# Optimization experiments

Hardware: AMD Instinct MI355X
Metric: run time of the kernel (lower is better)

Reference implementation:

```python
import jax, jax.numpy as jnp
import numpy as np

# Model dims
C = 16          # in_channels / d_model
D_INNER = 64    # expand * C, expand = 64 // C = 4
HEADDIM = 4
NHEADS = D_INNER // HEADDIM   # 16
D_STATE = 64
D_CONV = 4
CONV_DIM = D_INNER + 2 * D_STATE        # 192 (x, B, C streams)
D_IN_PROJ = 2 * D_INNER + 2 * D_STATE + NHEADS  # 272 (z, xBC, dt)
# Input volume
BSZ, DD, HH, WW = 8, 32, 16, 16
L = DD * HH * WW  # 8192, multiple of 256 -> exact adaptive max pool
POOL = 256


def setup_inputs():
    key = jax.random.key(0)
    ks = jax.random.split(key, 10)
    x = jax.random.normal(ks[0], (BSZ, C, DD, HH, WW), jnp.float32)
    # 3 independent Mamba2 blocks -> stack params with leading dim 3
    Win = jax.random.normal(ks[1], (3, D_IN_PROJ, C), jnp.float32) / np.sqrt(C).astype(np.float32)
    conv_w = jax.random.normal(ks[2], (3, CONV_DIM, D_CONV), jnp.float32) / np.sqrt(D_CONV).astype(np.float32)
    conv_b = jax.random.normal(ks[3], (3, CONV_DIM), jnp.float32) * 0.1
    dt_bias = jax.random.normal(ks[4], (3, NHEADS), jnp.float32) * 0.5
    A_log = jnp.log(jax.random.uniform(ks[5], (3, NHEADS), jnp.float32, minval=1.0, maxval=16.0))
    Dp = jax.random.normal(ks[6], (3, NHEADS), jnp.float32) * 0.5 + 1.0
    norm_w = jnp.ones((3, D_INNER), jnp.float32)
    Wout = jax.random.normal(ks[7], (3, C, D_INNER), jnp.float32) / np.sqrt(D_INNER).astype(np.float32)
    gamma = jnp.ones((3, C), jnp.float32)
    beta = jnp.zeros((3, C), jnp.float32)
    lin_w = jax.random.normal(ks[8], (3, 1, C), jnp.float32) / np.sqrt(C).astype(np.float32)
    lin_b = jnp.zeros((3, 1), jnp.float32)
    return dict(x=x, Win=Win, conv_w=conv_w, conv_b=conv_b, dt_bias=dt_bias,
                A_log=A_log, Dp=Dp, norm_w=norm_w, Wout=Wout,
                gamma=gamma, beta=beta, lin_w=lin_w, lin_b=lin_b)


def _mamba2(u, Win, conv_w, conv_b, dt_bias, A_log, Dp, norm_w, Wout):
    """Mamba2 block: u (B, L, C) -> (B, L, C). ngroups=1, rmsnorm gated."""
    B, Lx, _ = u.shape
    zxbcdt = jnp.einsum('blc,pc->blp', u, Win)  # (B, L, 272)
    z = zxbcdt[..., :D_INNER]
    xBC = zxbcdt[..., D_INNER:D_INNER + CONV_DIM]
    dt = jax.nn.softplus(zxbcdt[..., D_INNER + CONV_DIM:] + dt_bias)  # (B, L, H)
    # causal depthwise conv over time
    conv = jax.lax.conv_general_dilated(
        jnp.transpose(xBC, (0, 2, 1)), conv_w[:, None, :], (1,),
        [(D_CONV - 1, 0)], feature_group_count=CONV_DIM)
    xBC = jax.nn.silu(jnp.transpose(conv, (0, 2, 1)) + conv_b)
    xh = xBC[..., :D_INNER].reshape(B, Lx, NHEADS, HEADDIM)
    Bm = xBC[..., D_INNER:D_INNER + D_STATE]   # (B, L, N)
    Cm = xBC[..., D_INNER + D_STATE:]          # (B, L, N)
    A = -jnp.exp(A_log)                        # (H,)
    dA = jnp.exp(dt * A)                       # (B, L, H)
    dtx = dt[..., None] * xh                   # (B, L, H, P)

    def step(S, inp):
        dA_t, dtx_t, B_t, C_t = inp
        S = S * dA_t[:, :, None, None] + dtx_t[..., None] * B_t[:, None, None, :]
        y_t = jnp.einsum('bhpn,bn->bhp', S, C_t)
        return S, y_t

    S0 = jnp.zeros((B, NHEADS, HEADDIM, D_STATE), u.dtype)
    xs = (jnp.moveaxis(dA, 1, 0), jnp.moveaxis(dtx, 1, 0),
          jnp.moveaxis(Bm, 1, 0), jnp.moveaxis(Cm, 1, 0))
    _, ys = jax.lax.scan(step, S0, xs)                       # (L, B, H, P)
    y = jnp.moveaxis(ys, 0, 1) + Dp[None, None, :, None] * xh
    y = y.reshape(B, Lx, D_INNER) * jax.nn.silu(z)           # gate first
    y = y * jax.lax.rsqrt(jnp.mean(y * y, -1, keepdims=True) + 1e-5) * norm_w
    return jnp.einsum('bld,cd->blc', y, Wout)


def _proj_pool(y, gamma, beta, lw, lb):
    """ReLU -> BatchNorm1d (batch stats) -> Linear(C,1) -> AdaptiveMaxPool1d(256)."""
    B, Lx, _ = y.shape
    v = jax.nn.relu(y.reshape(-1, C))
    mu = jnp.mean(v, 0)
    var = jnp.mean((v - mu) ** 2, 0)
    v = (v - mu) * jax.lax.rsqrt(var + 1e-5) * gamma + beta
    s = (v @ lw.T + lb).reshape(B, Lx)
    return jnp.max(s.reshape(B, POOL, Lx // POOL), -1)  # (B, 256)


def reference(x, Win, conv_w, conv_b, dt_bias, A_log, Dp, norm_w, Wout,
              gamma, beta, lin_w, lin_b):
    B, Cc, Dd, Hh, Ww = x.shape
    Lx = Dd * Hh * Ww
    fD = jnp.transpose(x.reshape(B, Cc, Lx), (0, 2, 1))
    fH = jnp.transpose(jnp.transpose(x, (0, 1, 3, 4, 2)).reshape(B, Cc, Lx), (0, 2, 1))
    fW = jnp.transpose(jnp.transpose(x, (0, 1, 4, 2, 3)).reshape(B, Cc, Lx), (0, 2, 1))
    seqs = jnp.stack([fD, fH, fW], 0)  # (3, B, L, C)
    ys = jax.vmap(_mamba2)(seqs, Win, conv_w, conv_b, dt_bias, A_log, Dp, norm_w, Wout)
    pooled = jax.vmap(_proj_pool)(ys, gamma, beta, lin_w, lin_b)  # (3, B, 256)
    return jnp.concatenate([pooled[0], pooled[1], pooled[2]], -1)[:, None, :]  # (B,1,768)
```

## Files before the change

### kernel.cpp

```cpp
#include <hip/hip_runtime.h>
#include <math.h>

#define CONVD 192
#define NC 128
#define PW 32
#define LOG2E 1.4426950408889634f
#define LN2f  0.69314718055994531f

#define OFF_DST   0u
#define OFF_CHA   4194304u
#define OFF_YS    4210688u
#define OFF_PART  5259264u
#define PD        5292032u

#define XSW(m, t)   ((m) * 64 + (((((t) >> 2) ^ ((m) & 15)) & 15) << 2) + ((t) & 3))
#define XSW4(m, tq) ((m) * 64 + ((((tq) ^ ((m) & 15)) & 15) << 2))

__device__ __forceinline__ float fast_silu(float x) {
    float e = __builtin_amdgcn_exp2f(-x * LOG2E);
    return x * __builtin_amdgcn_rcpf(1.f + e);
}
__device__ __forceinline__ float fast_softplus(float x) {
    if (x > 20.f) return x;
    float e = __builtin_amdgcn_exp2f(x * LOG2E);
    return LN2f * __builtin_amdgcn_logf(1.f + e);
}

template<int CTRL>
__device__ __forceinline__ float dpp_ror_add(float x) {
    int yi = __builtin_amdgcn_update_dpp(0, __float_as_int(x), CTRL, 0xf, 0xf, false);
    return x + __int_as_float(yi);
}
__device__ __forceinline__ float rowsum16(float x) {
    x = dpp_ror_add<0x128>(x);
    x = dpp_ror_add<0x124>(x);
    x = dpp_ror_add<0x122>(x);
    x = dpp_ror_add<0x121>(x);
    return x;
}

template<int NT>
__device__ __forceinline__ void stage_u(
    const float* __restrict__ x, float* u_s, int b, int l0, int dir, int tid)
{
    for (int i = tid; i < 67 * 16; i += NT) {
        int pos = i >> 4, c = i & 15;
        int l = l0 + pos - 3;
        float v = 0.f;
        if (l >= 0) {
            if (dir == 0) {
                v = x[(b * 16 + c) * 8192 + l];
            } else if (dir == 1) {
                int h = l >> 9, w = (l >> 5) & 15, d = l & 31;
                v = x[(((b * 16 + c) * 32 + d) * 16 + h) * 16 + w];
            } else {
                int w = l >> 9, d = (l >> 4) & 31, h = l & 15;
                v = x[(((b * 16 + c) * 32 + d) * 16 + h) * 16 + w];
            }
        }
        u_s[pos * 17 + c] = v;
    }
}

__global__ __launch_bounds__(512, 6) void k_delta(
    const float* __restrict__ x, const float* __restrict__ Win,
    const float* __restrict__ convw, const float* __restrict__ convb,
    const float* __restrict__ dtb, const float* __restrict__ A_log,
    float* __restrict__ ws, int dir0, int dslm)
{
    __shared__ float u_s[67 * 17];
    __shared__ float xh_c[4096];
    __shared__ float Bs[4096];
    __shared__ float dts[16 * 65];
    __shared__ float wbuf[16 * 65];
    const int tid = threadIdx.x;
    const int ck = blockIdx.x;
    const int b = blockIdx.y;
    const int dir = dir0 + blockIdx.z;
    float* base = ws + (size_t)(dslm * blockIdx.z) * PD;
    float* Dst = base + OFF_DST;
    float* chA = base + OFF_CHA;
    const int l0 = ck * 64;

    stage_u<512>(x, u_s, b, l0, dir, tid);
    __syncthreads();

    const int lane = tid & 63;
    const int wv = __builtin_amdgcn_readfirstlane(tid >> 6);

    float u[16], uh[16];
    {
        const float* ur = &u_s[(lane + 3) * 17];
        #pragma unroll
        for (int k = 0; k < 16; k++) u[k] = ur[k];
        const float* uhr = &u_s[(lane < 3 ? lane : 0) * 17];
        #pragma unroll
        for (int k = 0; k < 16; k++) uh[k] = uhr[k];
    }

    for (int i = 0; i < 18; i++) {
        const int g = wv * 18 + i;
        const int col = (g < 128) ? (64 + g) : (256 + (g - 128));
        const float* wp = Win + (size_t)(dir * 272 + col) * 16;
        float acc = 0.f, hacc = 0.f;
        #pragma unroll
        for (int k = 0; k < 16; k++) {
            acc += u[k] * wp[k];
            hacc += uh[k] * wp[k];
        }
        if (col < 256) {
            const int ch = col - 64;
            float v1 = __shfl_up(acc, 1);
            float v2 = __shfl_up(acc, 2);
            float v3 = __shfl_up(acc, 3);
            float h0 = __shfl(hacc, 0);
            float h1 = __shfl(hacc, 1);
            float h2 = __shfl(hacc, 2);
            float m1 = (lane >= 1) ? v1 : h2;
            float m2 = (lane >= 2) ? v2 : ((lane == 0) ? h1 : h2);
            float m3 = (lane >= 3) ? v3 : ((lane == 0) ? h0 : ((lane == 1) ? h1 : h2));
            const float* cwp = convw + (size_t)(dir * CONVD + ch) * 4;
            float conv = convb[dir * CONVD + ch]
                       + cwp[0] * m3 + cwp[1] * m2 + cwp[2] * m1 + cwp[3] * acc;
            float xv = fast_silu(conv);
            if (ch < 64) xh_c[XSW(ch, lane)] = xv;
            else         Bs[XSW(ch - 64, lane)] = xv;
        } else {
            const int h = col - 256;
            dts[h * 65 + lane] = fast_softplus(acc + dtb[dir * 16 + h]);
        }
    }
    __syncthreads();

    for (int h = wv; h < 16; h += 8) {
        float A2 = -expf(A_log[dir * 16 + h]) * LOG2E;
        float dtv = dts[h * 65 + lane];
        float v = dtv * A2;
        #pragma unroll
        for (int off = 1; off < 64; off <<= 1) {
            float o = __shfl_up(v, off, 64);
            if (lane >= off) v += o;
        }
        float tot = __shfl(v, 63, 64);
        wbuf[h * 65 + lane] = __builtin_amdgcn_exp2f(tot - v) * dtv;
        if (lane == 63) chA[(b * 16 + h) * 128 + ck] = __builtin_amdgcn_exp2f(tot);
    }
    __syncthreads();

    for (int j = tid; j < 4096; j += 512) {
        int hp = j >> 6, t = j & 63;
        xh_c[XSW(hp, t)] *= wbuf[(hp >> 2) * 65 + t];
    }
    __syncthreads();

    if (tid < 256) {
        const int hp4 = tid >> 4, n4 = tid & 15;
        float a[4][4] = {};
        for (int tq = 0; tq < 16; tq++) {
            float4 xv[4], bv[4];
            #pragma unroll
            for (int i2 = 0; i2 < 4; i2++) {
                xv[i2] = *(const float4*)&xh_c[XSW4(4 * hp4 + i2, tq)];
                bv[i2] = *(const float4*)&Bs[XSW4(4 * n4 + i2, tq)];
            }
            #pragma unroll
            for (int i2 = 0; i2 < 4; i2++)
                #pragma unroll
                for (int j2 = 0; j2 < 4; j2++)
                    a[i2][j2] += xv[i2].x * bv[j2].x + xv[i2].y * bv[j2].y
                               + xv[i2].z * bv[j2].z + xv[i2].w * bv[j2].w;
        }
        #pragma unroll
        for (int i2 = 0; i2 < 4; i2++) {
            int hp = 4 * hp4 + i2;
            int h = hp >> 2, p = hp & 3;
            *(float4*)(Dst + ((size_t)((b * 16 + h) * 128 + ck)) * 256 + p * 64 + 4 * n4) =
                make_float4(a[i2][0], a[i2][1], a[i2][2], a[i2][3]);
        }
    }
}

__global__ __launch_bounds__(64) void k_chunk_scan(
    float* __restrict__ ws, int dslm)
{
    float* base = ws + (size_t)(dslm * blockIdx.z) * PD;
    float* Dst = base + OFF_DST;
    const float* chA = base + OFF_CHA;
    const int bh = blockIdx.x >> 2;
    const int elem = (blockIdx.x & 3) * 64 + threadIdx.x;
    float S = 0.f;
    for (int k0 = 0; k0 < NC; k0 += 8) {
        float d[8], av[8];
        #pragma unroll
        for (int j = 0; j < 8; j++) {
            d[j] = Dst[((size_t)(bh * 128 + k0 + j)) * 256 + elem];
            av[j] = chA[bh * 128 + k0 + j];
        }
        #pragma unroll
        for (int j = 0; j < 8; j++) {
            Dst[((size_t)(bh * 128 + k0 + j)) * 256 + elem] = S;
            S = av[j] * S + d[j];
        }
    }
}

__global__ __launch_bounds__(512, 4) void k_out_epi(
    const float* __restrict__ x, const float* __restrict__ Win,
    const float* __restrict__ convw, const float* __restrict__ convb,
    const float* __restrict__ dtb, const float* __restrict__ A_log,
    const float* __restrict__ Dp, const float* __restrict__ normw,
    const float* __restrict__ Wout, float* __restrict__ ws, int dir0, int dslm)
{
    __shared__ float SinT[64 * 65];
    __shared__ float xh_c[4096];
    __shared__ float Bz[4096];
    __shared__ float Cy[4352];
    __shared__ float uW[67 * 17];
    __shared__ float dts[16 * 65];
    __shared__ float ct2l[16 * 65];
    __shared__ float Dps[16];
    __shared__ float red[4][34];
    float* base = ws + (size_t)(dslm * blockIdx.z) * PD;
    const float* Dst = base + OFF_DST;
    float* ys        = base + OFF_YS;
    float* partials  = base + OFF_PART;
    const int dir = dir0 + blockIdx.z;
    const int tid = threadIdx.x;
    const int b = blockIdx.y;
    const int ck = blockIdx.x;
    const int l0 = ck * 64;
    const int tg = tid & 255;
    const int t4 = tg >> 4, x4 = tg & 15;
    const int grp = tid >> 8;
    const int lane = tid & 63;
    const int wv = __builtin_amdgcn_readfirstlane(tid >> 6);

    stage_u<512>(x, uW, b, l0, dir, tid);
    for (int j = tid; j < 1024; j += 512) {
        int hp = j >> 4, n4 = (j & 15) << 2;
        int h = hp >> 2, p = hp & 3;
        float4 sv = *(const float4*)(Dst + ((size_t)((b * 16 + h) * 128 + ck)) * 256 + p * 64 + n4);
        SinT[(n4 + 0) * 65 + hp] = sv.x;
        SinT[(n4 + 1) * 65 + hp] = sv.y;
        SinT[(n4 + 2) * 65 + hp] = sv.z;
        SinT[(n4 + 3) * 65 + hp] = sv.w;
    }
    if (tid < 16) Dps[tid] = Dp[dir * 16 + tid];
    __syncthreads();

    float u[16], uh[16];
    {
        const float* ur = &uW[(lane + 3) * 17];
        #pragma unroll
        for (int k = 0; k < 16; k++) u[k] = ur[k];
        const float* uhr = &uW[(lane < 3 ? lane : 0) * 17];
        #pragma unroll
        for (int k = 0; k < 16; k++) uh[k] = uhr[k];
    }

    for (int i = 0; i < 26; i++) {
        const int col = 64 + wv * 26 + i;
        const float* wp = Win + (size_t)(dir * 272 + col) * 16;
        float acc = 0.f, hacc = 0.f;
        #pragma unroll
        for (int k = 0; k < 16; k++) {
            acc += u[k] * wp[k];
            hacc += uh[k] * wp[k];
        }
        if (col < 256) {
            const int ch = col - 64;
            float v1 = __shfl_up(acc, 1);
            float v2 = __shfl_up(acc, 2);
            float v3 = __shfl_up(acc, 3);
            float h0 = __shfl(hacc, 0);
            float h1 = __shfl(hacc, 1);
            float h2 = __shfl(hacc, 2);
            float m1 = (lane >= 1) ? v1 : h2;
            float m2 = (lane >= 2) ? v2 : ((lane == 0) ? h1 : h2);
            float m3 = (lane >= 3) ? v3 : ((lane == 0) ? h0 : ((lane == 1) ? h1 : h2));
            const float* cwp = convw + (size_t)(dir * CONVD + ch) * 4;
            float conv = convb[dir * CONVD + ch]
                       + cwp[0] * m3 + cwp[1] * m2 + cwp[2] * m1 + cwp[3] * acc;
            float xv = fast_silu(conv);
            if (ch < 64)       xh_c[XSW(ch, lane)] = xv;
            else if (ch < 128) Bz[XSW(ch - 64, lane)] = xv;
            else               Cy[XSW(ch - 128, lane)] = xv;
        } else {
            const int h = col - 256;
            dts[h * 65 + lane] = fast_softplus(acc + dtb[dir * 16 + h]);
        }
    }
    __syncthreads();

    for (int h = wv; h < 16; h += 8) {
        float A2 = -expf(A_log[dir * 16 + h]) * LOG2E;
        float dtv = dts[h * 65 + lane];
        float v = dtv * A2;
        #pragma unroll
        for (int off = 1; off < 64; off <<= 1) {
            float o = __shfl_up(v, off, 64);
            if (lane >= off) v += o;
        }
        ct2l[h * 65 + lane] = v;
    }
    __syncthreads();

    float G_[4][4] = {}, CS_[4][4] = {};
    for (int n = 0; n < 64; n++) {
        float4 cr4 = *(const float4*)&Cy[XSW4(n, t4)];
        float4 br4 = *(const float4*)&Bz[XSW4(n, x4)];
        float cr[4] = {cr4.x, cr4.y, cr4.z, cr4.w};
        float br[4] = {br4.x, br4.y, br4.z, br4.w};
        float sn[4];
        #pragma unroll
        for (int q = 0; q < 4; q++) sn[q] = SinT[n * 65 + 4 * x4 + q];
        #pragma unroll
        for (int r = 0; r < 4; r++)
            #pragma unroll
            for (int q = 0; q < 4; q++) {
                G_[r][q] += cr[r] * br[q];
                CS_[r][q] += cr[r] * sn[q];
            }
    }
    __syncthreads();

    for (int i = 0; i < 8; i++) {
        const int col = wv * 8 + i;
        const float* wp = Win + (size_t)(dir * 272 + col) * 16;
        float acc = 0.f;
        #pragma unroll
        for (int k = 0; k < 16; k++) acc += u[k] * wp[k];
        Bz[XSW(col, lane)] = acc;
    }
    __syncthreads();
    for (int j = tid; j < 1024; j += 512) {
        int c = j >> 6, d = j & 63;
        uW[c * 65 + d] = Wout[dir * 1024 + j] * normw[dir * 64 + d];
    }
    __syncthreads();

    float* yv = Cy;
    const int tbase = 4 * t4;
    #pragma unroll 1
    for (int hh = 0; hh < 8; hh++) {
        const int h = 8 * grp + hh;
        float ctt[4], ect[4];
        #pragma unroll
        for (int r = 0; r < 4; r++) {
            ctt[r] = ct2l[h * 65 + tbase + r];
            ect[r] = __builtin_amdgcn_exp2f(ctt[r]);
        }
        float acc[4][4] = {};
        #pragma unroll
        for (int q = 0; q < 4; q++) {
            int s = 4 * x4 + q;
            float cs_ = ct2l[h * 65 + s];
            float dtq = dts[h * 65 + s];
            float xv[4];
            #pragma unroll
            for (int p = 0; p < 4; p++) {
                int m = 4 * h + p;
                xv[p] = xh_c[m * 64 + (((x4 ^ (m & 15)) & 15) << 2) + q];
            }
            #pragma unroll
            for (int r = 0; r < 4; r++) {
                float e = __builtin_amdgcn_exp2f(ctt[r] - cs_);
                e = (s <= tbase + r) ? e : 0.f;
                float w = G_[r][q] * e * dtq;
                #pragma unroll
                for (int p = 0; p < 4; p++) acc[r][p] += w * xv[p];
            }
        }
        if (x4 == h) {
            #pragma unroll
            for (int r = 0; r < 4; r++)
                #pragma unroll
                for (int p = 0; p < 4; p++)
                    acc[r][p] += ect[r] * CS_[r][p];
        }
        #pragma unroll
        for (int r = 0; r < 4; r++)
            #pragma unroll
            for (int p = 0; p < 4; p++)
                acc[r][p] = rowsum16(acc[r][p]);
        float outv = acc[0][0];
        #pragma unroll
        for (int r = 0; r < 4; r++)
            #pragma unroll
            for (int p = 0; p < 4; p++)
                if (r || p) outv = (x4 == r * 4 + p) ? acc[r][p] : outv;
        const int row = tbase + (x4 >> 2);
        const int pp = x4 & 3;
        yv[(row * 4 + pp) * 17 + h] = outv;
    }
    __syncthreads();

    float os[4];
    const int row = tid >> 2;
    const int p = tid & 3;
    if (tid < 256) {
        float gg[16], sumsq = 0.f;
        #pragma unroll
        for (int h = 0; h < 16; h++) {
            float yval = yv[(row * 4 + p) * 17 + h];
            int m = 4 * h + p;
            int ax = m * 64 + ((((row >> 2) ^ (m & 15)) & 15) << 2) + (row & 3);
            float xh = xh_c[ax];
            float zv = Bz[ax];
            float val = (yval + Dps[h] * xh) * fast_silu(zv);
            gg[h] = val;
            sumsq += val * val;
        }
        sumsq += __shfl_xor(sumsq, 1);
        sumsq += __shfl_xor(sumsq, 2);
        float rms = rsqrtf(sumsq * (1.f / 64.f) + 1e-5f);

        float oc[16];
        #pragma unroll
        for (int c = 0; c < 16; c++) {
            float a = 0.f;
            #pragma unroll
            for (int h = 0; h < 16; h++) a += gg[h] * uW[c * 65 + 4 * h + p];
            oc[c] = a;
        }
        #pragma unroll
        for (int c = 0; c < 16; c++) {
            oc[c] += __shfl_xor(oc[c], 1);
            oc[c] += __shfl_xor(oc[c], 2);
        }
        #pragma unroll
        for (int i2 = 0; i2 < 4; i2++) {
            float a0 = (p == 0) ? oc[i2] : oc[4 + i2];
            float a1 = (p == 2) ? oc[8 + i2] : oc[12 + i2];
            os[i2] = (((p & 2) == 0) ? a0 : a1) * rms;
        }
        size_t bl = (size_t)(b * 8192 + l0 + row);
        *(float4*)(ys + bl * 16 + 4 * p) = make_float4(os[0], os[1], os[2], os[3]);

        float bs[4], bq[4];
        #pragma unroll
        for (int i2 = 0; i2 < 4; i2++) {
            float vv = fmaxf(os[i2], 0.f);
            bs[i2] = vv;
            bq[i2] = vv * vv;
        }
        #pragma unroll
        for (int off = 4; off < 64; off <<= 1) {
            #pragma unroll
            for (int i2 = 0; i2 < 4; i2++) {
                bs[i2] += __shfl_xor(bs[i2], off);
                bq[i2] += __shfl_xor(bq[i2], off);
            }
        }
        const int wlane = tid & 63, wvid = tid >> 6;
        if (wlane < 4) {
            #pragma unroll
            for (int i2 = 0; i2 < 4; i2++) {
                red[wvid][4 * wlane + i2] = bs[i2];
                red[wvid][16 + 4 * wlane + i2] = bq[i2];
            }
        }
    }
    __syncthreads();
    if (tid < 32) {
        float a = red[0][tid] + red[1][tid] + red[2][tid] + red[3][tid];
        partials[((size_t)(b * 128 + ck)) * 32 + tid] = a;
    }
}

__global__ __launch_bounds__(256) void k_pool_bn(
    const float* __restrict__ gamma, const float* __restrict__ beta,
    const float* __restrict__ lin_w, const float* __restrict__ lin_b,
    float* __restrict__ ws, float* __restrict__ out, int dir0, int dslm)
{
    float* base = ws + (size_t)(dslm * blockIdx.z) * PD;
    const float* ys = base + OFF_YS;
    const float* partials = base + OFF_PART;
    const int dir = dir0 + blockIdx.z;
    const int tid = threadIdx.x;
    __shared__ float red[8][33];
    __shared__ float cf[18];
    {
        int c = tid & 31, ks = tid >> 5;
        float a = 0.f;
        for (int k = ks * 128; k < ks * 128 + 128; k++) a += partials[k * 32 + c];
        red[ks][c] = a;
    }
    __syncthreads();
    if (tid < 32) {
        float a = 0.f;
        #pragma unroll
        for (int s2 = 1; s2 < 8; s2++) a += red[s2][tid];
        red[0][tid] += a;
    }
    __syncthreads();
    if (tid == 0) {
        float off = lin_b[dir];
        for (int c = 0; c < 16; c++) {
            float mu = red[0][c] * (1.f / 65536.f);
            float var = red[0][16 + c] * (1.f / 65536.f) - mu * mu;
            float inv = rsqrtf(var + 1e-5f);
            float coef = inv * gamma[dir * 16 + c] * lin_w[dir * 16 + c];
            cf[c] = coef;
            off += beta[dir * 16 + c] * lin_w[dir * 16 + c] - mu * coef;
        }
        cf[16] = off;
    }
    __syncthreads();

    const int b = blockIdx.x >> 3;
    const int jg = blockIdx.x & 7;
    const int j = jg * 32 + (tid >> 3);
    const int sub = tid & 7;
    float m = -3.4e38f;
    #pragma unroll
    for (int r = 0; r < 4; r++) {
        int l = j * PW + 8 * r + sub;
        const float* rowp = ys + (size_t)(b * 8192 + l) * 16;
        float sv = cf[16];
        #pragma unroll
        for (int k = 0; k < 4; k++) {
            float4 v4 = *(const float4*)(rowp + 4 * k);
            sv += fmaxf(v4.x, 0.f) * cf[4 * k] + fmaxf(v4.y, 0.f) * cf[4 * k + 1]
                + fmaxf(v4.z, 0.f) * cf[4 * k + 2] + fmaxf(v4.w, 0.f) * cf[4 * k + 3];
        }
        m = fmaxf(m, sv);
    }
    m = fmaxf(m, __shfl_xor(m, 1));
    m = fmaxf(m, __shfl_xor(m, 2));
    m = fmaxf(m, __shfl_xor(m, 4));
    if (sub == 0) out[b * 768 + dir * 256 + j] = m;
}

extern "C" void kernel_launch(void* const* d_in, const int* in_sizes, int n_in,
                              void* d_out, int out_size, void* d_ws, size_t ws_size,
                              hipStream_t stream) {
    const float* x     = (const float*)d_in[0];
    const float* Win   = (const float*)d_in[1];
    const float* convw = (const float*)d_in[2];
    const float* convb = (const float*)d_in[3];
    const float* dtb   = (const float*)d_in[4];
    const float* Alog  = (const float*)d_in[5];
    const float* Dp    = (const float*)d_in[6];
    const float* normw = (const float*)d_in[7];
    const float* Wout  = (const float*)d_in[8];
    const float* gamma = (const float*)d_in[9];
    const float* beta  = (const float*)d_in[10];
    const float* linw  = (const float*)d_in[11];
    const float* linb  = (const float*)d_in[12];
    float* out = (float*)d_out;
    float* ws = (float*)d_ws;

    const bool batched = ws_size >= (size_t)3 * PD * 4;
    const int nz = batched ? 3 : 1;
    const int dslm = batched ? 1 : 0;
    const int nloop = batched ? 1 : 3;

    for (int d0 = 0; d0 < nloop; ++d0) {
        k_delta<<<dim3(128, 8, nz), dim3(512), 0, stream>>>(
            x, Win, convw, convb, dtb, Alog, ws, d0, dslm);
        k_chunk_scan<<<dim3(512, 1, nz), dim3(64), 0, stream>>>(ws, dslm);
        k_out_epi<<<dim3(128, 8, nz), dim3(512), 0, stream>>>(
            x, Win, convw, convb, dtb, Alog, Dp, normw, Wout, ws, d0, dslm);
        k_pool_bn<<<dim3(64, 1, nz), dim3(256), 0, stream>>>(
            gamma, beta, linw, linb, ws, out, d0, dslm);
    }
}
```

Before: 380.8 us.

## Split G/CS accumulation across thread groups and use recursive-halving reduce

Result: faster. 356.1 us (-6.5%).

```diff
diff --git a/kernel.cpp b/kernel.cpp
--- a/kernel.cpp
+++ b/kernel.cpp
@@ -24,19 +24,6 @@
     if (x > 20.f) return x;
     float e = __builtin_amdgcn_exp2f(x * LOG2E);
     return LN2f * __builtin_amdgcn_logf(1.f + e);
-}
-
-template<int CTRL>
-__device__ __forceinline__ float dpp_ror_add(float x) {
-    int yi = __builtin_amdgcn_update_dpp(0, __float_as_int(x), CTRL, 0xf, 0xf, false);
-    return x + __int_as_float(yi);
-}
-__device__ __forceinline__ float rowsum16(float x) {
-    x = dpp_ror_add<0x128>(x);
-    x = dpp_ror_add<0x124>(x);
-    x = dpp_ror_add<0x122>(x);
-    x = dpp_ror_add<0x121>(x);
-    return x;
 }
 
 template<int NT>
@@ -216,8 +203,8 @@
     __shared__ float Bz[4096];
     __shared__ float Cy[4352];
     __shared__ float uW[67 * 17];
-    __shared__ float dts[16 * 65];
-    __shared__ float ct2l[16 * 65];
+    __shared__ float dts[16 * 68];
+    __shared__ float ct2l[16 * 68];
     __shared__ float Dps[16];
     __shared__ float red[4][34];
     float* base = ws + (size_t)(dslm * blockIdx.z) * PD;
@@ -287,42 +274,70 @@
             else               Cy[XSW(ch - 128, lane)] = xv;
         } else {
             const int h = col - 256;
-            dts[h * 65 + lane] = fast_softplus(acc + dtb[dir * 16 + h]);
+            dts[h * 68 + lane] = fast_softplus(acc + dtb[dir * 16 + h]);
         }
     }
     __syncthreads();
 
     for (int h = wv; h < 16; h += 8) {
         float A2 = -expf(A_log[dir * 16 + h]) * LOG2E;
-        float dtv = dts[h * 65 + lane];
+        float dtv = dts[h * 68 + lane];
         float v = dtv * A2;
         #pragma unroll
         for (int off = 1; off < 64; off <<= 1) {
             float o = __shfl_up(v, off, 64);
             if (lane >= off) v += o;
         }
-        ct2l[h * 65 + lane] = v;
+        ct2l[h * 68 + lane] = v;
     }
     __syncthreads();
 
     float G_[4][4] = {}, CS_[4][4] = {};
-    for (int n = 0; n < 64; n++) {
-        float4 cr4 = *(const float4*)&Cy[XSW4(n, t4)];
-        float4 br4 = *(const float4*)&Bz[XSW4(n, x4)];
-        float cr[4] = {cr4.x, cr4.y, cr4.z, cr4.w};
-        float br[4] = {br4.x, br4.y, br4.z, br4.w};
-        float sn[4];
-        #pragma unroll
-        for (int q = 0; q < 4; q++) sn[q] = SinT[n * 65 + 4 * x4 + q];
-        #pragma unroll
-        for (int r = 0; r < 4; r++)
-            #pragma unroll
-            for (int q = 0; q < 4; q++) {
-                G_[r][q] += cr[r] * br[q];
-                CS_[r][q] += cr[r] * sn[q];
-            }
-    }
-    __syncthreads();
+    if (grp == 0) {
+        for (int n = 0; n < 64; n++) {
+            float4 cr4 = *(const float4*)&Cy[XSW4(n, t4)];
+            float4 br4 = *(const float4*)&Bz[XSW4(n, x4)];
+            float cr[4] = {cr4.x, cr4.y, cr4.z, cr4.w};
+            float br[4] = {br4.x, br4.y, br4.z, br4.w};
+            #pragma unroll
+            for (int r = 0; r < 4; r++)
+                #pragma unroll
+                for (int q = 0; q < 4; q++)
+                    G_[r][q] += cr[r] * br[q];
+        }
+    } else {
+        for (int n = 0; n < 64; n++) {
+            float4 cr4 = *(const float4*)&Cy[XSW4(n, t4)];
+            float cr[4] = {cr4.x, cr4.y, cr4.z, cr4.w};
+            float sn[4];
+            #pragma unroll
+            for (int q = 0; q < 4; q++) sn[q] = SinT[n * 65 + 4 * x4 + q];
+            #pragma unroll
+            for (int r = 0; r < 4; r++)
+                #pragma unroll
+                for (int q = 0; q < 4; q++)
+                    CS_[r][q] += cr[r] * sn[q];
+        }
+    }
+    __syncthreads();
+
+    if (grp == 0) {
+        #pragma unroll
+        for (int k = 0; k < 16; k++) Cy[k * 257 + tg] = G_[k >> 2][k & 3];
+    } else if (x4 < 8) {
+        const int idx = t4 * 8 + x4;
+        #pragma unroll
+        for (int k = 0; k < 16; k++) SinT[k * 129 + idx] = CS_[k >> 2][k & 3];
+    }
+    __syncthreads();
+    if (grp == 1) {
+        #pragma unroll
+        for (int k = 0; k < 16; k++) G_[k >> 2][k & 3] = Cy[k * 257 + tg];
+    } else if (x4 < 8) {
+        const int idx = t4 * 8 + x4;
+        #pragma unroll
+        for (int k = 0; k < 16; k++) CS_[k >> 2][k & 3] = SinT[k * 129 + idx];
+    }
 
     for (int i = 0; i < 8; i++) {
         const int col = wv * 8 + i;
@@ -332,7 +347,6 @@
         for (int k = 0; k < 16; k++) acc += u[k] * wp[k];
         Bz[XSW(col, lane)] = acc;
     }
-    __syncthreads();
     for (int j = tid; j < 1024; j += 512) {
         int c = j >> 6, d = j & 63;
         uW[c * 65 + d] = Wout[dir * 1024 + j] * normw[dir * 64 + d];
@@ -344,18 +358,22 @@
     #pragma unroll 1
     for (int hh = 0; hh < 8; hh++) {
         const int h = 8 * grp + hh;
-        float ctt[4], ect[4];
-        #pragma unroll
-        for (int r = 0; r < 4; r++) {
-            ctt[r] = ct2l[h * 65 + tbase + r];
-            ect[r] = __builtin_amdgcn_exp2f(ctt[r]);
-        }
-        float acc[4][4] = {};
+        const float* ctp = &ct2l[h * 68];
+        const float* dtp = &dts[h * 68];
+        float4 ctt4 = *(const float4*)&ctp[tbase];
+        const float ctt[4] = {ctt4.x, ctt4.y, ctt4.z, ctt4.w};
+        float ect[4];
+        #pragma unroll
+        for (int r = 0; r < 4; r++) ect[r] = __builtin_amdgcn_exp2f(ctt[r]);
+        float4 cs4 = *(const float4*)&ctp[4 * x4];
+        float4 dt4 = *(const float4*)&dtp[4 * x4];
+        float v[16] = {0.f, 0.f, 0.f, 0.f, 0.f, 0.f, 0.f, 0.f,
+                       0.f, 0.f, 0.f, 0.f, 0.f, 0.f, 0.f, 0.f};
         #pragma unroll
         for (int q = 0; q < 4; q++) {
-            int s = 4 * x4 + q;
-            float cs_ = ct2l[h * 65 + s];
-            float dtq = dts[h * 65 + s];
+            const int s = 4 * x4 + q;
+            float csq = (q == 0) ? cs4.x : (q == 1) ? cs4.y : (q == 2) ? cs4.z : cs4.w;
+            float dtq = (q == 0) ? dt4.x : (q == 1) ? dt4.y : (q == 2) ? dt4.z : dt4.w;
             float xv[4];
             #pragma unroll
             for (int p = 0; p < 4; p++) {
@@ -364,11 +382,10 @@
             }
             #pragma unroll
             for (int r = 0; r < 4; r++) {
-                float e = __builtin_amdgcn_exp2f(ctt[r] - cs_);
-                e = (s <= tbase + r) ? e : 0.f;
-                float w = G_[r][q] * e * dtq;
+                float e = __builtin_amdgcn_exp2f(ctt[r] - csq);
+                float w = (s <= tbase + r) ? (G_[r][q] * dtq) * e : 0.f;
                 #pragma unroll
-                for (int p = 0; p < 4; p++) acc[r][p] += w * xv[p];
+                for (int p = 0; p < 4; p++) v[4 * r + p] += w * xv[p];
             }
         }
         if (x4 == h) {
@@ -376,22 +393,33 @@
             for (int r = 0; r < 4; r++)
                 #pragma unroll
                 for (int p = 0; p < 4; p++)
-                    acc[r][p] += ect[r] * CS_[r][p];
-        }
-        #pragma unroll
-        for (int r = 0; r < 4; r++)
-            #pragma unroll
-            for (int p = 0; p < 4; p++)
-                acc[r][p] = rowsum16(acc[r][p]);
-        float outv = acc[0][0];
-        #pragma unroll
-        for (int r = 0; r < 4; r++)
-            #pragma unroll
-            for (int p = 0; p < 4; p++)
-                if (r || p) outv = (x4 == r * 4 + p) ? acc[r][p] : outv;
+                    v[4 * r + p] += ect[r] * CS_[r][p];
+        }
+        #pragma unroll
+        for (int j = 0; j < 8; j++) {
+            float a = (x4 & 8) ? v[j + 8] : v[j];
+            float s_ = (x4 & 8) ? v[j] : v[j + 8];
+            v[j] = a + __shfl_xor(s_, 8);
+        }
+        #pragma unroll
+        for (int j = 0; j < 4; j++) {
+            float a = (x4 & 4) ? v[j + 4] : v[j];
+            float s_ = (x4 & 4) ? v[j] : v[j + 4];
+            v[j] = a + __shfl_xor(s_, 4);
+        }
+        #pragma unroll
+        for (int j = 0; j < 2; j++) {
+            float a = (x4 & 2) ? v[j + 2] : v[j];
+            float s_ = (x4 & 2) ? v[j] : v[j + 2];
+            v[j] = a + __shfl_xor(s_, 2);
+        }
+        {
+            float a = (x4 & 1) ? v[1] : v[0];
+            float s_ = (x4 & 1) ? v[0] : v[1];
+            v[0] = a + __shfl_xor(s_, 1);
+        }
         const int row = tbase + (x4 >> 2);
-        const int pp = x4 & 3;
-        yv[(row * 4 + pp) * 17 + h] = outv;
+        yv[(row * 4 + (x4 & 3)) * 17 + h] = v[0];
     }
     __syncthreads();
 
```
